# Performance work log

Hardware: AMD Instinct MI355X
Metric: run time of the kernel (lower is better)

## Reference

```python
import jax, jax.numpy as jnp
import numpy as np

EPS = 1e-5  # BatchNorm1d default eps
HEADS = 4


def _batchnorm(x, gamma, beta):
    # BatchNorm1d applied per graph: stats over node axis (axis=1), biased var (training mode)
    mean = x.mean(axis=1, keepdims=True)
    var = x.var(axis=1, keepdims=True)
    return gamma * (x - mean) * jax.lax.rsqrt(var + EPS) + beta


def setup_inputs() -> dict:
    key = jax.random.key(0)
    ks = jax.random.split(key, 8)
    B, N, F_in, C = 4, 4096, 128, 64
    inputs = jax.random.normal(ks[0], (B, N, F_in), jnp.float32)
    # sparse-ish adjacency (avg degree ~16); only used for non-emptiness check since conv=None
    adj = (jax.random.uniform(ks[1], (B, N, N)) < 0.004).astype(jnp.float32)
    s = lambda k, shp, fan: jax.random.normal(k, shp, jnp.float32) / np.sqrt(fan)
    return dict(
        inputs=inputs, adj=adj,
        Wp=s(ks[2], (C, F_in), F_in), bp=jnp.zeros((C,), jnp.float32),      # project Linear
        Wqkv=s(ks[3], (3 * C, C), C), bqkv=jnp.zeros((3 * C,), jnp.float32),  # MHA in_proj
        Wo=s(ks[4], (C, C), C), bo=jnp.zeros((C,), jnp.float32),            # MHA out_proj
        g2=jnp.ones((C,), jnp.float32), b2=jnp.zeros((C,), jnp.float32),    # norm2 (BatchNorm)
        W1=s(ks[5], (2 * C, C), C), b1=jnp.zeros((2 * C,), jnp.float32),    # MLP Linear 1
        W2=s(ks[6], (C, 2 * C), 2 * C), b2m=jnp.zeros((C,), jnp.float32),   # MLP Linear 2
        g3=jnp.ones((C,), jnp.float32), b3=jnp.zeros((C,), jnp.float32),    # norm3 (BatchNorm)
    )


def reference(inputs, adj, Wp, bp, Wqkv, bqkv, Wo, bo, g2, b2, W1, b1, W2, b2m, g3, b3):
    B, N, _ = inputs.shape
    C = Wp.shape[0]
    Dh = C // HEADS
    # project in_features -> out_features
    x = jnp.einsum('bnf,cf->bnc', inputs, Wp) + bp
    # GPSConv with conv=None: only the global multi-head self-attention branch runs
    qkv = jnp.einsum('bnc,dc->bnd', x, Wqkv) + bqkv
    q, k, v = jnp.split(qkv, 3, axis=-1)
    rs = lambda t: t.reshape(B, N, HEADS, Dh)
    q, k, v = rs(q), rs(k), rs(v)
    scores = jnp.einsum('bnhd,bmhd->bhnm', q, k) / np.sqrt(Dh).astype(np.float32)
    attn = jax.nn.softmax(scores, axis=-1)
    o = jnp.einsum('bhnm,bmhd->bnhd', attn, v).reshape(B, N, C)
    h = jnp.einsum('bnc,oc->bno', o, Wo) + bo
    # residual + norm2
    h = _batchnorm(h + x, g2, b2)
    # out = h (sum of single-branch hs); out = out + mlp(out); norm3
    mlp = jnp.einsum('bnk,ck->bnc',
                     jax.nn.relu(jnp.einsum('bnc,kc->bnk', h, W1) + b1),
                     W2) + b2m
    out = _batchnorm(h + mlp, g3, b3)
    # wrapper applies tanh (edge_index non-empty)
    return jnp.tanh(out)
```

## Files before the change

kernel.cpp:

```cpp
#include <hip/hip_runtime.h>
#include <hip/hip_bf16.h>

constexpr int NN = 4096;
constexpr int CC = 64;
constexpr int NH = 4;
constexpr int DH = 16;
constexpr int KSPLIT = 4;

typedef _Float16 f16x4 __attribute__((ext_vector_type(4)));
typedef float f32x4 __attribute__((ext_vector_type(4)));

#define QSCALE 0.36067376022224085f
#define L2E2   2.8853900817779268f

#if defined(__has_builtin)
#if __has_builtin(__builtin_amdgcn_exp2f)
#define FAST_EXP2(x) __builtin_amdgcn_exp2f(x)
#endif
#if __has_builtin(__builtin_amdgcn_rcpf)
#define FAST_RCP(x) __builtin_amdgcn_rcpf(x)
#endif
#endif
#ifndef FAST_EXP2
#define FAST_EXP2(x) exp2f(x)
#endif
#ifndef FAST_RCP
#define FAST_RCP(x) (1.0f / (x))
#endif

__device__ __forceinline__ float fast_tanh(float x) {
  const float t = FAST_EXP2(x * L2E2);
  return fmaf(-2.f, FAST_RCP(t + 1.f), 1.f);
}

__global__ __launch_bounds__(256) void proj_qkv_k(
    const float* __restrict__ inp, const float* __restrict__ Wp,
    const float* __restrict__ bp, const float* __restrict__ Wqkv,
    const float* __restrict__ bqkv, float* __restrict__ xout,
    _Float16* __restrict__ f16b)
{
  __shared__ __align__(16) float As[64][68];
  __shared__ __align__(16) float Xs[64][68];
  __shared__ __align__(16) float W2s[64][196];

  const int tid = threadIdx.x;
  const int rowbase = blockIdx.x * 64;
  const int r4 = (tid & 15) * 4;
  const int cg = (tid >> 4) * 4;
  const int cg2 = (tid >> 4) * 12;

  float acc[4][4];
  #pragma unroll
  for (int i = 0; i < 4; ++i)
    #pragma unroll
    for (int j = 0; j < 4; ++j) acc[i][j] = 0.f;

  for (int k0 = 0; k0 < 128; k0 += 64) {
    if (k0) __syncthreads();
    #pragma unroll
    for (int i = 0; i < 16; ++i) {
      int idx = tid + i * 256;
      int c2 = idx >> 6, kk = idx & 63;
      Xs[kk][c2] = Wp[(size_t)c2 * 128 + k0 + kk];
    }
    #pragma unroll
    for (int i = 0; i < 16; ++i) {
      int idx = tid + i * 256;
      int r = idx >> 6, kk = idx & 63;
      As[kk][r] = inp[(size_t)(rowbase + r) * 128 + k0 + kk];
    }
    __syncthreads();
    #pragma unroll 4
    for (int kk = 0; kk < 64; ++kk) {
      const float4 a = *(const float4*)&As[kk][r4];
      const float4 w4 = *(const float4*)&Xs[kk][cg];
      const float av[4] = {a.x, a.y, a.z, a.w};
      const float wv[4] = {w4.x, w4.y, w4.z, w4.w};
      #pragma unroll
      for (int ri = 0; ri < 4; ++ri)
        #pragma unroll
        for (int ci = 0; ci < 4; ++ci)
          acc[ri][ci] = fmaf(av[ri], wv[ci], acc[ri][ci]);
    }
  }

  float xv[4][4];
  #pragma unroll
  for (int ri = 0; ri < 4; ++ri)
    #pragma unroll
    for (int j = 0; j < 4; ++j) {
      xv[ri][j] = acc[ri][j] + bp[cg + j];
      xout[(size_t)(rowbase + r4 + ri) * CC + cg + j] = xv[ri][j];
    }

  __syncthreads();
  #pragma unroll
  for (int ri = 0; ri < 4; ++ri)
    #pragma unroll
    for (int j = 0; j < 4; ++j)
      Xs[cg + j][r4 + ri] = xv[ri][j];
  #pragma unroll
  for (int i = 0; i < 48; ++i) {
    int idx = tid + i * 256;
    int c2 = idx >> 6, kk = idx & 63;
    W2s[kk][c2] = Wqkv[(size_t)c2 * 64 + kk];
  }
  __syncthreads();

  float acc2[4][12];
  #pragma unroll
  for (int i = 0; i < 4; ++i)
    #pragma unroll
    for (int j = 0; j < 12; ++j) acc2[i][j] = 0.f;

  #pragma unroll 4
  for (int kk = 0; kk < 64; ++kk) {
    const float4 a = *(const float4*)&Xs[kk][r4];
    const float av[4] = {a.x, a.y, a.z, a.w};
    #pragma unroll
    for (int cj = 0; cj < 3; ++cj) {
      const float4 w4 = *(const float4*)&W2s[kk][cg2 + cj * 4];
      const float wv[4] = {w4.x, w4.y, w4.z, w4.w};
      #pragma unroll
      for (int ri = 0; ri < 4; ++ri)
        #pragma unroll
        for (int ci = 0; ci < 4; ++ci)
          acc2[ri][cj * 4 + ci] = fmaf(av[ri], wv[ci], acc2[ri][cj * 4 + ci]);
    }
  }

  #pragma unroll
  for (int ri = 0; ri < 4; ++ri) {
    const int row = rowbase + r4 + ri;
    const int n = row & (NN - 1);
    const int bq = (row >> 12) * NH;
    #pragma unroll
    for (int j = 0; j < 12; ++j) {
      float v = acc2[ri][j] + bqkv[cg2 + j];
      const int c2 = cg2 + j;
      const int which = c2 >> 6;
      const int hc = c2 & 63;
      const int bh = bq + (hc >> 4);
      const int d = hc & 15;
      if (which == 0) v *= QSCALE;
      if (which < 2)
        f16b[(size_t)which * 1048576 + ((size_t)bh * NN + n) * DH + d] = (_Float16)v;
      else
        f16b[2097152 + ((size_t)bh * DH + d) * NN + n] = (_Float16)v;
    }
  }
}

__global__ __launch_bounds__(256, 8) void attn_k(
    const _Float16* __restrict__ qb, const _Float16* __restrict__ kb,
    const _Float16* __restrict__ vtb, float* __restrict__ po,
    float* __restrict__ rs)
{
  __shared__ _Float16 Kl[64][20];
  __shared__ _Float16 Vl[16][72];

  const int bid = blockIdx.x;
  const int xcd = bid & 7;
  const int rest = bid >> 3;
  const int bh = 2 * xcd + (rest & 1);
  const int ks = (rest >> 1) & 3;
  const int n0 = (rest >> 3) * 128;
  const int tid = threadIdx.x;
  const int w = tid >> 6;
  const int l = tid & 63;
  const int g = l >> 4, i = l & 15;
  const int qbase = n0 + w * 32;
  const int kbeg = ks * (NN / KSPLIT);
  const int kend = kbeg + NN / KSPLIT;

  const _Float16* __restrict__ qhp = qb + (size_t)bh * NN * DH;
  const _Float16* __restrict__ khp = kb + (size_t)bh * NN * DH;
  const _Float16* __restrict__ vhp = vtb + (size_t)bh * DH * NN;

  const f16x4 qfA = *(const f16x4*)(qhp + (size_t)(qbase + i) * DH + 4 * g);
  const f16x4 qfB = *(const f16x4*)(qhp + (size_t)(qbase + 16 + i) * DH + 4 * g);

  f32x4 oA = {0.f, 0.f, 0.f, 0.f}, oB = {0.f, 0.f, 0.f, 0.f};
  const f32x4 zz = {0.f, 0.f, 0.f, 0.f};
  float rsA = 0.f, rsB = 0.f;

  const int srow = tid >> 2, spart = tid & 3;
  const int sd = tid >> 4, scol = (tid & 15) * 4;

  for (int c0 = kbeg; c0 < kend; c0 += 64) {
    __syncthreads();
    *(f16x4*)&Kl[srow][spart * 4] =
        *(const f16x4*)(khp + (size_t)(c0 + srow) * DH + spart * 4);
    *(f16x4*)&Vl[sd][scol] =
        *(const f16x4*)(vhp + (size_t)sd * NN + c0 + scol);
    __syncthreads();

    #pragma unroll
    for (int kk = 0; kk < 64; kk += 16) {
      const f16x4 kf = *(const f16x4*)&Kl[kk + i][4 * g];
      const f16x4 vf = *(const f16x4*)&Vl[i][kk + 4 * g];
      f32x4 sA = __builtin_amdgcn_mfma_f32_16x16x16f16(kf, qfA, zz, 0, 0, 0);
      f32x4 sB = __builtin_amdgcn_mfma_f32_16x16x16f16(kf, qfB, zz, 0, 0, 0);
      const float a0 = FAST_EXP2(sA[0]), a1 = FAST_EXP2(sA[1]),
                  a2 = FAST_EXP2(sA[2]), a3 = FAST_EXP2(sA[3]);
      const float b0 = FAST_EXP2(sB[0]), b1 = FAST_EXP2(sB[1]),
                  b2 = FAST_EXP2(sB[2]), b3 = FAST_EXP2(sB[3]);
      rsA += (a0 + a1) + (a2 + a3);
      rsB += (b0 + b1) + (b2 + b3);
      const auto alo = __builtin_amdgcn_cvt_pkrtz(a0, a1);
      const auto ahi = __builtin_amdgcn_cvt_pkrtz(a2, a3);
      const auto blo = __builtin_amdgcn_cvt_pkrtz(b0, b1);
      const auto bhi = __builtin_amdgcn_cvt_pkrtz(b2, b3);
      f16x4 pA, pB;
      pA[0] = (_Float16)alo[0]; pA[1] = (_Float16)alo[1];
      pA[2] = (_Float16)ahi[0]; pA[3] = (_Float16)ahi[1];
      pB[0] = (_Float16)blo[0]; pB[1] = (_Float16)blo[1];
      pB[2] = (_Float16)bhi[0]; pB[3] = (_Float16)bhi[1];
      oA = __builtin_amdgcn_mfma_f32_16x16x16f16(pA, vf, oA, 0, 0, 0);
      oB = __builtin_amdgcn_mfma_f32_16x16x16f16(pB, vf, oB, 0, 0, 0);
    }
  }

  rsA += __shfl_xor(rsA, 16); rsA += __shfl_xor(rsA, 32);
  rsB += __shfl_xor(rsB, 16); rsB += __shfl_xor(rsB, 32);

  float* __restrict__ pob = po + (size_t)(ks * 16 + bh) * NN * DH;
  #pragma unroll
  for (int r = 0; r < 4; ++r) {
    const int ql = 4 * g + r;
    pob[(size_t)(qbase + ql) * DH + i] = oA[r];
    pob[(size_t)(qbase + 16 + ql) * DH + i] = oB[r];
  }
  if (g == 0) {
    float* __restrict__ rsb = rs + (size_t)(ks * 16 + bh) * NN;
    rsb[qbase + i] = rsA;
    rsb[qbase + 16 + i] = rsB;
  }
}

__global__ __launch_bounds__(256) void wo_red_k(
    const float* __restrict__ po, const float* __restrict__ rs,
    const float* __restrict__ Wo, const float* __restrict__ bo,
    const float* __restrict__ xin, float* __restrict__ out)
{
  __shared__ __align__(16) float As[64][68];
  __shared__ __align__(16) float Ws[64][68];
  __shared__ float Linv[64][4];

  const int tid = threadIdx.x;
  const int rowbase = blockIdx.x * 64;
  const int r4 = (tid & 15) * 4;
  const int cg = (tid >> 4) * 4;

  {
    const int r = tid & 63, hb = tid >> 6;
    const int row = rowbase + r;
    const int bh = (row >> 12) * NH + hb;
    const int n = row & (NN - 1);
    const float s = rs[(size_t)bh * NN + n] + rs[(size_t)(16 + bh) * NN + n] +
                    rs[(size_t)(32 + bh) * NN + n] + rs[(size_t)(48 + bh) * NN + n];
    Linv[r][hb] = 1.f / s;
  }
  #pragma unroll
  for (int i = 0; i < 16; ++i) {
    int idx = tid + i * 256;
    int c2 = idx >> 6, kk = idx & 63;
    Ws[kk][c2] = Wo[(size_t)c2 * 64 + kk];
  }
  __syncthreads();
  #pragma unroll
  for (int i = 0; i < 16; ++i) {
    int idx = tid + i * 256;
    int r = idx >> 6, kk = idx & 63;
    const int row = rowbase + r;
    const int bh = (row >> 12) * NH + (kk >> 4);
    const int n = row & (NN - 1);
    const int d = kk & 15;
    const size_t base = (((size_t)bh * NN + n) * DH) + d;
    const float v = po[base] + po[base + 1048576] +
                    po[base + 2097152] + po[base + 3145728];
    As[kk][r] = v * Linv[r][kk >> 4];
  }
  __syncthreads();

  float acc[4][4];
  #pragma unroll
  for (int i = 0; i < 4; ++i)
    #pragma unroll
    for (int j = 0; j < 4; ++j) acc[i][j] = 0.f;

  #pragma unroll 4
  for (int kk = 0; kk < 64; ++kk) {
    const float4 a = *(const float4*)&As[kk][r4];
    const float4 w4 = *(const float4*)&Ws[kk][cg];
    const float av[4] = {a.x, a.y, a.z, a.w};
    const float wv[4] = {w4.x, w4.y, w4.z, w4.w};
    #pragma unroll
    for (int ri = 0; ri < 4; ++ri)
      #pragma unroll
      for (int ci = 0; ci < 4; ++ci)
        acc[ri][ci] = fmaf(av[ri], wv[ci], acc[ri][ci]);
  }

  #pragma unroll
  for (int ri = 0; ri < 4; ++ri) {
    const int row = rowbase + r4 + ri;
    #pragma unroll
    for (int j = 0; j < 4; ++j) {
      const int c = cg + j;
      out[(size_t)row * CC + c] =
          acc[ri][j] + bo[c] + xin[(size_t)row * CC + c];
    }
  }
}

__global__ __launch_bounds__(256) void mlp_k(
    const float* __restrict__ hf, const float* __restrict__ W1,
    const float* __restrict__ b1, const float* __restrict__ W2,
    const float* __restrict__ b2m, float* __restrict__ out)
{
  __shared__ __align__(16) float As[64][68];
  __shared__ __align__(16) float Wbuf[8704];
  __shared__ __align__(16) float Ts[128][68];

  const int tid = threadIdx.x;
  const int rowbase = blockIdx.x * 64;
  const int r4 = (tid & 15) * 4;
  const int cg8 = (tid >> 4) * 8;
  const int cg4 = (tid >> 4) * 4;

  #pragma unroll
  for (int i = 0; i < 32; ++i) {
    int idx = tid + i * 256;
    int c2 = idx >> 6, kk = idx & 63;
    Wbuf[kk * 132 + c2] = W1[(size_t)c2 * 64 + kk];
  }
  #pragma unroll
  for (int i = 0; i < 16; ++i) {
    int idx = tid + i * 256;
    int r = idx >> 6, kk = idx & 63;
    As[kk][r] = hf[(size_t)(rowbase + r) * CC + kk];
  }
  __syncthreads();

  float acc1[4][8];
  #pragma unroll
  for (int i = 0; i < 4; ++i)
    #pragma unroll
    for (int j = 0; j < 8; ++j) acc1[i][j] = 0.f;

  #pragma unroll 4
  for (int kk = 0; kk < 64; ++kk) {
    const float4 a = *(const float4*)&As[kk][r4];
    const float av[4] = {a.x, a.y, a.z, a.w};
    #pragma unroll
    for (int cj = 0; cj < 2; ++cj) {
      const float4 w4 = *(const float4*)&Wbuf[kk * 132 + cg8 + cj * 4];
      const float wv[4] = {w4.x, w4.y, w4.z, w4.w};
      #pragma unroll
      for (int ri = 0; ri < 4; ++ri)
        #pragma unroll
        for (int ci = 0; ci < 4; ++ci)
          acc1[ri][cj * 4 + ci] = fmaf(av[ri], wv[ci], acc1[ri][cj * 4 + ci]);
    }
  }
  #pragma unroll
  for (int ri = 0; ri < 4; ++ri)
    #pragma unroll
    for (int j = 0; j < 8; ++j)
      Ts[cg8 + j][r4 + ri] = fmaxf(acc1[ri][j] + b1[cg8 + j], 0.f);
  __syncthreads();

  #pragma unroll
  for (int i = 0; i < 32; ++i) {
    int idx = tid + i * 256;
    int c2 = idx >> 7, kk = idx & 127;
    Wbuf[kk * 68 + c2] = W2[(size_t)c2 * 128 + kk];
  }
  __syncthreads();

  float acc2[4][4];
  #pragma unroll
  for (int i = 0; i < 4; ++i)
    #pragma unroll
    for (int j = 0; j < 4; ++j) acc2[i][j] = 0.f;

  #pragma unroll 4
  for (int kk = 0; kk < 128; ++kk) {
    const float4 a = *(const float4*)&Ts[kk][r4];
    const float4 w4 = *(const float4*)&Wbuf[kk * 68 + cg4];
    const float av[4] = {a.x, a.y, a.z, a.w};
    const float wv[4] = {w4.x, w4.y, w4.z, w4.w};
    #pragma unroll
    for (int ri = 0; ri < 4; ++ri)
      #pragma unroll
      for (int ci = 0; ci < 4; ++ci)
        acc2[ri][ci] = fmaf(av[ri], wv[ci], acc2[ri][ci]);
  }

  #pragma unroll
  for (int ri = 0; ri < 4; ++ri) {
    const int row = rowbase + r4 + ri;
    #pragma unroll
    for (int j = 0; j < 4; ++j) {
      const int c = cg4 + j;
      out[(size_t)row * CC + c] = acc2[ri][j] + b2m[c] + As[c][r4 + ri];
    }
  }
}

__global__ __launch_bounds__(256) void bn4_k(
    const float* __restrict__ in, const float* __restrict__ g,
    const float* __restrict__ b, float* __restrict__ out, int do_tanh)
{
  const int bb = blockIdx.x >> 4;
  const int c4 = (blockIdx.x & 15) * 4;
  const float* __restrict__ base = in + (size_t)bb * NN * CC + c4;
  const int tid = threadIdx.x;

  float4 s = {0, 0, 0, 0}, sq = {0, 0, 0, 0};
  #pragma unroll
  for (int i = 0; i < 16; ++i) {
    const float4 v = *(const float4*)&base[(size_t)(tid + i * 256) * CC];
    s.x += v.x; s.y += v.y; s.z += v.z; s.w += v.w;
    sq.x = fmaf(v.x, v.x, sq.x); sq.y = fmaf(v.y, v.y, sq.y);
    sq.z = fmaf(v.z, v.z, sq.z); sq.w = fmaf(v.w, v.w, sq.w);
  }
  #pragma unroll
  for (int off = 32; off; off >>= 1) {
    s.x += __shfl_down(s.x, off); s.y += __shfl_down(s.y, off);
    s.z += __shfl_down(s.z, off); s.w += __shfl_down(s.w, off);
    sq.x += __shfl_down(sq.x, off); sq.y += __shfl_down(sq.y, off);
    sq.z += __shfl_down(sq.z, off); sq.w += __shfl_down(sq.w, off);
  }
  __shared__ float red[4][8];
  const int wv = tid >> 6;
  if ((tid & 63) == 0) {
    red[wv][0] = s.x; red[wv][1] = s.y; red[wv][2] = s.z; red[wv][3] = s.w;
    red[wv][4] = sq.x; red[wv][5] = sq.y; red[wv][6] = sq.z; red[wv][7] = sq.w;
  }
  __syncthreads();
  float scale[4], shift[4];
  #pragma unroll
  for (int j = 0; j < 4; ++j) {
    const float ts = red[0][j] + red[1][j] + red[2][j] + red[3][j];
    const float tq = red[0][4 + j] + red[1][4 + j] + red[2][4 + j] + red[3][4 + j];
    const float mean = ts * (1.f / NN);
    const float var = tq * (1.f / NN) - mean * mean;
    const float rstd = rsqrtf(var + 1e-5f);
    scale[j] = g[c4 + j] * rstd;
    shift[j] = b[c4 + j] - mean * scale[j];
  }
  float* __restrict__ ob = out + (size_t)bb * NN * CC + c4;
  #pragma unroll
  for (int i = 0; i < 16; ++i) {
    const size_t idx = (size_t)(tid + i * 256) * CC;
    const float4 v = *(const float4*)&base[idx];
    float4 o;
    o.x = v.x * scale[0] + shift[0];
    o.y = v.y * scale[1] + shift[1];
    o.z = v.z * scale[2] + shift[2];
    o.w = v.w * scale[3] + shift[3];
    if (do_tanh) {
      o.x = fast_tanh(o.x); o.y = fast_tanh(o.y);
      o.z = fast_tanh(o.z); o.w = fast_tanh(o.w);
    }
    *(float4*)&ob[idx] = o;
  }
}

extern "C" void kernel_launch(void* const* d_in, const int* in_sizes, int n_in,
                              void* d_out, int out_size, void* d_ws, size_t ws_size,
                              hipStream_t stream)
{
  const float* inp  = (const float*)d_in[0];
  const float* Wp   = (const float*)d_in[2];
  const float* bp   = (const float*)d_in[3];
  const float* Wqkv = (const float*)d_in[4];
  const float* bqkv = (const float*)d_in[5];
  const float* Wo   = (const float*)d_in[6];
  const float* bo   = (const float*)d_in[7];
  const float* g2   = (const float*)d_in[8];
  const float* b2   = (const float*)d_in[9];
  const float* W1   = (const float*)d_in[10];
  const float* b1   = (const float*)d_in[11];
  const float* W2   = (const float*)d_in[12];
  const float* b2m  = (const float*)d_in[13];
  const float* g3   = (const float*)d_in[14];
  const float* b3   = (const float*)d_in[15];

  float* w = (float*)d_ws;
  float* x    = w;
  float* qkvA = w + 1048576;
  float* hf   = w + 2621440;
  float* pf   = w + 3670016;
  float* poW  = w + 4718592;
  float* rsW  = w + 8912896;

  _Float16* f16b = (_Float16*)qkvA;

  proj_qkv_k<<<dim3(256), dim3(256), 0, stream>>>(inp, Wp, bp, Wqkv, bqkv, x, f16b);
  attn_k<<<dim3(2048), dim3(256), 0, stream>>>(f16b, f16b + 1048576,
                                               f16b + 2097152, poW, rsW);
  wo_red_k<<<dim3(256), dim3(256), 0, stream>>>(poW, rsW, Wo, bo, x, hf);
  bn4_k<<<dim3(64), dim3(256), 0, stream>>>(hf, g2, b2, hf, 0);
  mlp_k<<<dim3(256), dim3(256), 0, stream>>>(hf, W1, b1, W2, b2m, pf);
  bn4_k<<<dim3(64), dim3(256), 0, stream>>>(pf, g3, b3, (float*)d_out, 1);
}
```

Baseline: 127.9 us.

## Double-buffer K/V tiles in attention kernel with register prefetch and larger chunks

The attention kernel now stages K and V in two LDS buffers of 128 keys each. The next chunk is loaded from global memory into registers while the current chunk is computed, then written to the other buffer. This replaces the two barriers per 64-key chunk with one barrier per 128-key chunk and uses 16-byte loads. The cost is twice the shared memory and more live registers, which may lower occupancy under the launch bound of 8 blocks.

Measured after the change: 206.6 us. 1.62x slower.

```diff
diff --git a/kernel.cpp b/kernel.cpp
--- a/kernel.cpp
+++ b/kernel.cpp
@@ -6,8 +6,10 @@
 constexpr int NH = 4;
 constexpr int DH = 16;
 constexpr int KSPLIT = 4;
+constexpr int KVB = 128;
 
 typedef _Float16 f16x4 __attribute__((ext_vector_type(4)));
+typedef _Float16 f16x8 __attribute__((ext_vector_type(8)));
 typedef float f32x4 __attribute__((ext_vector_type(4)));
 
 #define QSCALE 0.36067376022224085f
@@ -156,8 +158,8 @@
     const _Float16* __restrict__ vtb, float* __restrict__ po,
     float* __restrict__ rs)
 {
-  __shared__ _Float16 Kl[64][20];
-  __shared__ _Float16 Vl[16][72];
+  __shared__ _Float16 Kl[2][KVB][20];
+  __shared__ _Float16 Vl[2][16][KVB + 8];
 
   const int bid = blockIdx.x;
   const int xcd = bid & 7;
@@ -171,7 +173,6 @@
   const int g = l >> 4, i = l & 15;
   const int qbase = n0 + w * 32;
   const int kbeg = ks * (NN / KSPLIT);
-  const int kend = kbeg + NN / KSPLIT;
 
   const _Float16* __restrict__ qhp = qb + (size_t)bh * NN * DH;
   const _Float16* __restrict__ khp = kb + (size_t)bh * NN * DH;
@@ -184,21 +185,31 @@
   const f32x4 zz = {0.f, 0.f, 0.f, 0.f};
   float rsA = 0.f, rsB = 0.f;
 
-  const int srow = tid >> 2, spart = tid & 3;
-  const int sd = tid >> 4, scol = (tid & 15) * 4;
-
-  for (int c0 = kbeg; c0 < kend; c0 += 64) {
-    __syncthreads();
-    *(f16x4*)&Kl[srow][spart * 4] =
-        *(const f16x4*)(khp + (size_t)(c0 + srow) * DH + spart * 4);
-    *(f16x4*)&Vl[sd][scol] =
-        *(const f16x4*)(vhp + (size_t)sd * NN + c0 + scol);
-    __syncthreads();
-
-    #pragma unroll
-    for (int kk = 0; kk < 64; kk += 16) {
-      const f16x4 kf = *(const f16x4*)&Kl[kk + i][4 * g];
-      const f16x4 vf = *(const f16x4*)&Vl[i][kk + 4 * g];
+  const int sr = tid >> 1, sh = (tid & 1) * 8;
+  const int sd = tid >> 4, sc = (tid & 15) * 8;
+
+  {
+    const f16x8 kr = *(const f16x8*)(khp + (size_t)(kbeg + sr) * DH + sh);
+    const f16x8 vr = *(const f16x8*)(vhp + (size_t)sd * NN + kbeg + sc);
+    *(f16x8*)&Kl[0][sr][sh] = kr;
+    *(f16x8*)&Vl[0][sd][sc] = vr;
+  }
+  __syncthreads();
+
+  constexpr int NCH = (NN / KSPLIT) / KVB;
+  int cur = 0;
+  for (int c = 0; c < NCH; ++c) {
+    f16x8 kr, vr;
+    if (c + 1 < NCH) {
+      const int nx = kbeg + (c + 1) * KVB;
+      kr = *(const f16x8*)(khp + (size_t)(nx + sr) * DH + sh);
+      vr = *(const f16x8*)(vhp + (size_t)sd * NN + nx + sc);
+    }
+
+    #pragma unroll
+    for (int kk = 0; kk < KVB; kk += 16) {
+      const f16x4 kf = *(const f16x4*)&Kl[cur][kk + i][4 * g];
+      const f16x4 vf = *(const f16x4*)&Vl[cur][i][kk + 4 * g];
       f32x4 sA = __builtin_amdgcn_mfma_f32_16x16x16f16(kf, qfA, zz, 0, 0, 0);
       f32x4 sB = __builtin_amdgcn_mfma_f32_16x16x16f16(kf, qfB, zz, 0, 0, 0);
       const float a0 = FAST_EXP2(sA[0]), a1 = FAST_EXP2(sA[1]),
@@ -219,6 +230,13 @@
       oA = __builtin_amdgcn_mfma_f32_16x16x16f16(pA, vf, oA, 0, 0, 0);
       oB = __builtin_amdgcn_mfma_f32_16x16x16f16(pB, vf, oB, 0, 0, 0);
     }
+
+    if (c + 1 < NCH) {
+      *(f16x8*)&Kl[cur ^ 1][sr][sh] = kr;
+      *(f16x8*)&Vl[cur ^ 1][sd][sc] = vr;
+    }
+    __syncthreads();
+    cur ^= 1;
   }
 
   rsA += __shfl_xor(rsA, 16); rsA += __shfl_xor(rsA, 32);
```

## Shrink GEMM row tiles to 16 rows and read weights from global cache

Applied to the files above, without the earlier changes.

The projection/QKV, Wo-reduce and MLP kernels now each handle 16 rows per block instead of 64. Each thread computes one row against a few output columns and reads weights directly from global memory through the cache, no longer staging them transposed in LDS. This launches 1024 blocks instead of 256, filling more of the GPU's compute units for these small GEMMs and cutting LDS use and staging syncs. The cost is less register reuse, more global/L1 weight reads per FMA, and uncoalesced row-strided input loads.

Result: slower. 192.3 us (+50.4%).

```diff
diff --git a/kernel.cpp b/kernel.cpp
--- a/kernel.cpp
+++ b/kernel.cpp
@@ -33,121 +33,68 @@
   return fmaf(-2.f, FAST_RCP(t + 1.f), 1.f);
 }
 
-__global__ __launch_bounds__(256) void proj_qkv_k(
+__global__ __launch_bounds__(256, 4) void proj_qkv_k(
     const float* __restrict__ inp, const float* __restrict__ Wp,
     const float* __restrict__ bp, const float* __restrict__ Wqkv,
     const float* __restrict__ bqkv, float* __restrict__ xout,
     _Float16* __restrict__ f16b)
 {
-  __shared__ __align__(16) float As[64][68];
-  __shared__ __align__(16) float Xs[64][68];
-  __shared__ __align__(16) float W2s[64][196];
-
-  const int tid = threadIdx.x;
-  const int rowbase = blockIdx.x * 64;
-  const int r4 = (tid & 15) * 4;
-  const int cg = (tid >> 4) * 4;
-  const int cg2 = (tid >> 4) * 12;
-
-  float acc[4][4];
-  #pragma unroll
-  for (int i = 0; i < 4; ++i)
-    #pragma unroll
-    for (int j = 0; j < 4; ++j) acc[i][j] = 0.f;
-
-  for (int k0 = 0; k0 < 128; k0 += 64) {
-    if (k0) __syncthreads();
-    #pragma unroll
-    for (int i = 0; i < 16; ++i) {
-      int idx = tid + i * 256;
-      int c2 = idx >> 6, kk = idx & 63;
-      Xs[kk][c2] = Wp[(size_t)c2 * 128 + k0 + kk];
-    }
-    #pragma unroll
-    for (int i = 0; i < 16; ++i) {
-      int idx = tid + i * 256;
-      int r = idx >> 6, kk = idx & 63;
-      As[kk][r] = inp[(size_t)(rowbase + r) * 128 + k0 + kk];
-    }
-    __syncthreads();
-    #pragma unroll 4
-    for (int kk = 0; kk < 64; ++kk) {
-      const float4 a = *(const float4*)&As[kk][r4];
-      const float4 w4 = *(const float4*)&Xs[kk][cg];
-      const float av[4] = {a.x, a.y, a.z, a.w};
-      const float wv[4] = {w4.x, w4.y, w4.z, w4.w};
-      #pragma unroll
-      for (int ri = 0; ri < 4; ++ri)
-        #pragma unroll
-        for (int ci = 0; ci < 4; ++ci)
-          acc[ri][ci] = fmaf(av[ri], wv[ci], acc[ri][ci]);
-    }
-  }
-
-  float xv[4][4];
-  #pragma unroll
-  for (int ri = 0; ri < 4; ++ri)
-    #pragma unroll
-    for (int j = 0; j < 4; ++j) {
-      xv[ri][j] = acc[ri][j] + bp[cg + j];
-      xout[(size_t)(rowbase + r4 + ri) * CC + cg + j] = xv[ri][j];
-    }
-
+  __shared__ __align__(16) float Xs[16][68];
+
+  const int tid = threadIdx.x;
+  const int rowbase = blockIdx.x * 16;
+  const int r = tid & 15;
+  const int cg = tid >> 4;
+  const int row = rowbase + r;
+
+  float acc[4] = {0.f, 0.f, 0.f, 0.f};
+  const float* arow = inp + (size_t)row * 128;
+  #pragma unroll 8
+  for (int k = 0; k < 128; k += 4) {
+    const float4 a = *(const float4*)(arow + k);
+    #pragma unroll
+    for (int ci = 0; ci < 4; ++ci) {
+      const float4 w = *(const float4*)(Wp + (size_t)(cg * 4 + ci) * 128 + k);
+      acc[ci] = fmaf(a.x, w.x, fmaf(a.y, w.y, fmaf(a.z, w.z, fmaf(a.w, w.w, acc[ci]))));
+    }
+  }
+  #pragma unroll
+  for (int ci = 0; ci < 4; ++ci) {
+    const float v = acc[ci] + bp[cg * 4 + ci];
+    xout[(size_t)row * CC + cg * 4 + ci] = v;
+    Xs[r][cg * 4 + ci] = v;
+  }
   __syncthreads();
-  #pragma unroll
-  for (int ri = 0; ri < 4; ++ri)
-    #pragma unroll
-    for (int j = 0; j < 4; ++j)
-      Xs[cg + j][r4 + ri] = xv[ri][j];
-  #pragma unroll
-  for (int i = 0; i < 48; ++i) {
-    int idx = tid + i * 256;
-    int c2 = idx >> 6, kk = idx & 63;
-    W2s[kk][c2] = Wqkv[(size_t)c2 * 64 + kk];
-  }
-  __syncthreads();
-
-  float acc2[4][12];
-  #pragma unroll
-  for (int i = 0; i < 4; ++i)
-    #pragma unroll
-    for (int j = 0; j < 12; ++j) acc2[i][j] = 0.f;
-
+
+  float acc2[12];
+  #pragma unroll
+  for (int j = 0; j < 12; ++j) acc2[j] = 0.f;
+  const int cg2 = cg * 12;
   #pragma unroll 4
-  for (int kk = 0; kk < 64; ++kk) {
-    const float4 a = *(const float4*)&Xs[kk][r4];
-    const float av[4] = {a.x, a.y, a.z, a.w};
-    #pragma unroll
-    for (int cj = 0; cj < 3; ++cj) {
-      const float4 w4 = *(const float4*)&W2s[kk][cg2 + cj * 4];
-      const float wv[4] = {w4.x, w4.y, w4.z, w4.w};
-      #pragma unroll
-      for (int ri = 0; ri < 4; ++ri)
-        #pragma unroll
-        for (int ci = 0; ci < 4; ++ci)
-          acc2[ri][cj * 4 + ci] = fmaf(av[ri], wv[ci], acc2[ri][cj * 4 + ci]);
-    }
-  }
-
-  #pragma unroll
-  for (int ri = 0; ri < 4; ++ri) {
-    const int row = rowbase + r4 + ri;
-    const int n = row & (NN - 1);
-    const int bq = (row >> 12) * NH;
+  for (int k = 0; k < 64; k += 4) {
+    const float4 a = *(const float4*)&Xs[r][k];
     #pragma unroll
     for (int j = 0; j < 12; ++j) {
-      float v = acc2[ri][j] + bqkv[cg2 + j];
-      const int c2 = cg2 + j;
-      const int which = c2 >> 6;
-      const int hc = c2 & 63;
-      const int bh = bq + (hc >> 4);
-      const int d = hc & 15;
-      if (which == 0) v *= QSCALE;
-      if (which < 2)
-        f16b[(size_t)which * 1048576 + ((size_t)bh * NN + n) * DH + d] = (_Float16)v;
-      else
-        f16b[2097152 + ((size_t)bh * DH + d) * NN + n] = (_Float16)v;
-    }
+      const float4 w = *(const float4*)(Wqkv + (size_t)(cg2 + j) * 64 + k);
+      acc2[j] = fmaf(a.x, w.x, fmaf(a.y, w.y, fmaf(a.z, w.z, fmaf(a.w, w.w, acc2[j]))));
+    }
+  }
+
+  const int n = row & (NN - 1);
+  const int bq = (row >> 12) * NH;
+  #pragma unroll
+  for (int j = 0; j < 12; ++j) {
+    float v = acc2[j] + bqkv[cg2 + j];
+    const int c2 = cg2 + j;
+    const int which = c2 >> 6;
+    const int hc = c2 & 63;
+    const int bh = bq + (hc >> 4);
+    const int d = hc & 15;
+    if (which == 0) v *= QSCALE;
+    if (which < 2)
+      f16b[(size_t)which * 1048576 + ((size_t)bh * NN + n) * DH + d] = (_Float16)v;
+    else
+      f16b[2097152 + ((size_t)bh * DH + d) * NN + n] = (_Float16)v;
   }
 }
 
@@ -238,174 +185,103 @@
   }
 }
 
-__global__ __launch_bounds__(256) void wo_red_k(
+__global__ __launch_bounds__(256, 4) void wo_red_k(
     const float* __restrict__ po, const float* __restrict__ rs,
     const float* __restrict__ Wo, const float* __restrict__ bo,
     const float* __restrict__ xin, float* __restrict__ out)
 {
-  __shared__ __align__(16) float As[64][68];
-  __shared__ __align__(16) float Ws[64][68];
-  __shared__ float Linv[64][4];
-
-  const int tid = threadIdx.x;
-  const int rowbase = blockIdx.x * 64;
-  const int r4 = (tid & 15) * 4;
-  const int cg = (tid >> 4) * 4;
+  __shared__ __align__(16) float Xs[16][68];
+
+  const int tid = threadIdx.x;
+  const int rowbase = blockIdx.x * 16;
 
   {
-    const int r = tid & 63, hb = tid >> 6;
+    const int r = tid >> 4, kk4 = (tid & 15) * 4;
     const int row = rowbase + r;
-    const int bh = (row >> 12) * NH + hb;
     const int n = row & (NN - 1);
-    const float s = rs[(size_t)bh * NN + n] + rs[(size_t)(16 + bh) * NN + n] +
-                    rs[(size_t)(32 + bh) * NN + n] + rs[(size_t)(48 + bh) * NN + n];
-    Linv[r][hb] = 1.f / s;
-  }
-  #pragma unroll
-  for (int i = 0; i < 16; ++i) {
-    int idx = tid + i * 256;
-    int c2 = idx >> 6, kk = idx & 63;
-    Ws[kk][c2] = Wo[(size_t)c2 * 64 + kk];
+    const int bh = (row >> 12) * NH + (kk4 >> 4);
+    const int d0 = kk4 & 15;
+    const size_t base = ((size_t)bh * NN + n) * DH + d0;
+    const float4 p0 = *(const float4*)(po + base);
+    const float4 p1 = *(const float4*)(po + base + 1048576);
+    const float4 p2 = *(const float4*)(po + base + 2097152);
+    const float4 p3 = *(const float4*)(po + base + 3145728);
+    const size_t rb = (size_t)bh * NN + n;
+    const float sden = rs[rb] + rs[rb + 65536] + rs[rb + 131072] + rs[rb + 196608];
+    const float inv = 1.f / sden;
+    Xs[r][kk4 + 0] = (p0.x + p1.x + p2.x + p3.x) * inv;
+    Xs[r][kk4 + 1] = (p0.y + p1.y + p2.y + p3.y) * inv;
+    Xs[r][kk4 + 2] = (p0.z + p1.z + p2.z + p3.z) * inv;
+    Xs[r][kk4 + 3] = (p0.w + p1.w + p2.w + p3.w) * inv;
   }
   __syncthreads();
-  #pragma unroll
-  for (int i = 0; i < 16; ++i) {
-    int idx = tid + i * 256;
-    int r = idx >> 6, kk = idx & 63;
-    const int row = rowbase + r;
-    const int bh = (row >> 12) * NH + (kk >> 4);
-    const int n = row & (NN - 1);
-    const int d = kk & 15;
-    const size_t base = (((size_t)bh * NN + n) * DH) + d;
-    const float v = po[base] + po[base + 1048576] +
-                    po[base + 2097152] + po[base + 3145728];
-    As[kk][r] = v * Linv[r][kk >> 4];
-  }
-  __syncthreads();
-
-  float acc[4][4];
-  #pragma unroll
-  for (int i = 0; i < 4; ++i)
-    #pragma unroll
-    for (int j = 0; j < 4; ++j) acc[i][j] = 0.f;
-
+
+  const int r = tid & 15;
+  const int cg = tid >> 4;
+  const int row = rowbase + r;
+  float acc[4] = {0.f, 0.f, 0.f, 0.f};
   #pragma unroll 4
-  for (int kk = 0; kk < 64; ++kk) {
-    const float4 a = *(const float4*)&As[kk][r4];
-    const float4 w4 = *(const float4*)&Ws[kk][cg];
-    const float av[4] = {a.x, a.y, a.z, a.w};
-    const float wv[4] = {w4.x, w4.y, w4.z, w4.w};
-    #pragma unroll
-    for (int ri = 0; ri < 4; ++ri)
-      #pragma unroll
-      for (int ci = 0; ci < 4; ++ci)
-        acc[ri][ci] = fmaf(av[ri], wv[ci], acc[ri][ci]);
-  }
-
-  #pragma unroll
-  for (int ri = 0; ri < 4; ++ri) {
-    const int row = rowbase + r4 + ri;
-    #pragma unroll
-    for (int j = 0; j < 4; ++j) {
-      const int c = cg + j;
-      out[(size_t)row * CC + c] =
-          acc[ri][j] + bo[c] + xin[(size_t)row * CC + c];
-    }
-  }
-}
-
-__global__ __launch_bounds__(256) void mlp_k(
+  for (int k = 0; k < 64; k += 4) {
+    const float4 a = *(const float4*)&Xs[r][k];
+    #pragma unroll
+    for (int ci = 0; ci < 4; ++ci) {
+      const float4 w = *(const float4*)(Wo + (size_t)(cg * 4 + ci) * 64 + k);
+      acc[ci] = fmaf(a.x, w.x, fmaf(a.y, w.y, fmaf(a.z, w.z, fmaf(a.w, w.w, acc[ci]))));
+    }
+  }
+  #pragma unroll
+  for (int ci = 0; ci < 4; ++ci) {
+    const int c = cg * 4 + ci;
+    out[(size_t)row * CC + c] = acc[ci] + bo[c] + xin[(size_t)row * CC + c];
+  }
+}
+
+__global__ __launch_bounds__(256, 4) void mlp_k(
     const float* __restrict__ hf, const float* __restrict__ W1,
     const float* __restrict__ b1, const float* __restrict__ W2,
     const float* __restrict__ b2m, float* __restrict__ out)
 {
-  __shared__ __align__(16) float As[64][68];
-  __shared__ __align__(16) float Wbuf[8704];
-  __shared__ __align__(16) float Ts[128][68];
-
-  const int tid = threadIdx.x;
-  const int rowbase = blockIdx.x * 64;
-  const int r4 = (tid & 15) * 4;
-  const int cg8 = (tid >> 4) * 8;
-  const int cg4 = (tid >> 4) * 4;
-
-  #pragma unroll
-  for (int i = 0; i < 32; ++i) {
-    int idx = tid + i * 256;
-    int c2 = idx >> 6, kk = idx & 63;
-    Wbuf[kk * 132 + c2] = W1[(size_t)c2 * 64 + kk];
-  }
-  #pragma unroll
-  for (int i = 0; i < 16; ++i) {
-    int idx = tid + i * 256;
-    int r = idx >> 6, kk = idx & 63;
-    As[kk][r] = hf[(size_t)(rowbase + r) * CC + kk];
-  }
+  __shared__ __align__(16) float Ts[16][132];
+
+  const int tid = threadIdx.x;
+  const int rowbase = blockIdx.x * 16;
+  const int r = tid & 15;
+  const int cg = tid >> 4;
+  const int row = rowbase + r;
+  const float* hrow = hf + (size_t)row * CC;
+
+  float acc1[8];
+  #pragma unroll
+  for (int j = 0; j < 8; ++j) acc1[j] = 0.f;
+  const int cg8 = cg * 8;
+  #pragma unroll 4
+  for (int k = 0; k < 64; k += 4) {
+    const float4 a = *(const float4*)(hrow + k);
+    #pragma unroll
+    for (int j = 0; j < 8; ++j) {
+      const float4 w = *(const float4*)(W1 + (size_t)(cg8 + j) * 64 + k);
+      acc1[j] = fmaf(a.x, w.x, fmaf(a.y, w.y, fmaf(a.z, w.z, fmaf(a.w, w.w, acc1[j]))));
+    }
+  }
+  #pragma unroll
+  for (int j = 0; j < 8; ++j)
+    Ts[r][cg8 + j] = fmaxf(acc1[j] + b1[cg8 + j], 0.f);
   __syncthreads();
 
-  float acc1[4][8];
-  #pragma unroll
-  for (int i = 0; i < 4; ++i)
-    #pragma unroll
-    for (int j = 0; j < 8; ++j) acc1[i][j] = 0.f;
-
+  float acc2[4] = {0.f, 0.f, 0.f, 0.f};
   #pragma unroll 4
-  for (int kk = 0; kk < 64; ++kk) {
-    const float4 a = *(const float4*)&As[kk][r4];
-    const float av[4] = {a.x, a.y, a.z, a.w};
-    #pragma unroll
-    for (int cj = 0; cj < 2; ++cj) {
-      const float4 w4 = *(const float4*)&Wbuf[kk * 132 + cg8 + cj * 4];
-      const float wv[4] = {w4.x, w4.y, w4.z, w4.w};
-      #pragma unroll
-      for (int ri = 0; ri < 4; ++ri)
-        #pragma unroll
-        for (int ci = 0; ci < 4; ++ci)
-          acc1[ri][cj * 4 + ci] = fmaf(av[ri], wv[ci], acc1[ri][cj * 4 + ci]);
-    }
-  }
-  #pragma unroll
-  for (int ri = 0; ri < 4; ++ri)
-    #pragma unroll
-    for (int j = 0; j < 8; ++j)
-      Ts[cg8 + j][r4 + ri] = fmaxf(acc1[ri][j] + b1[cg8 + j], 0.f);
-  __syncthreads();
-
-  #pragma unroll
-  for (int i = 0; i < 32; ++i) {
-    int idx = tid + i * 256;
-    int c2 = idx >> 7, kk = idx & 127;
-    Wbuf[kk * 68 + c2] = W2[(size_t)c2 * 128 + kk];
-  }
-  __syncthreads();
-
-  float acc2[4][4];
-  #pragma unroll
-  for (int i = 0; i < 4; ++i)
-    #pragma unroll
-    for (int j = 0; j < 4; ++j) acc2[i][j] = 0.f;
-
-  #pragma unroll 4
-  for (int kk = 0; kk < 128; ++kk) {
-    const float4 a = *(const float4*)&Ts[kk][r4];
-    const float4 w4 = *(const float4*)&Wbuf[kk * 68 + cg4];
-    const float av[4] = {a.x, a.y, a.z, a.w};
-    const float wv[4] = {w4.x, w4.y, w4.z, w4.w};
-    #pragma unroll
-    for (int ri = 0; ri < 4; ++ri)
-      #pragma unroll
-      for (int ci = 0; ci < 4; ++ci)
-        acc2[ri][ci] = fmaf(av[ri], wv[ci], acc2[ri][ci]);
-  }
-
-  #pragma unroll
-  for (int ri = 0; ri < 4; ++ri) {
-    const int row = rowbase + r4 + ri;
-    #pragma unroll
-    for (int j = 0; j < 4; ++j) {
-      const int c = cg4 + j;
-      out[(size_t)row * CC + c] = acc2[ri][j] + b2m[c] + As[c][r4 + ri];
-    }
+  for (int k = 0; k < 128; k += 4) {
+    const float4 a = *(const float4*)&Ts[r][k];
+    #pragma unroll
+    for (int ci = 0; ci < 4; ++ci) {
+      const float4 w = *(const float4*)(W2 + (size_t)(cg * 4 + ci) * 128 + k);
+      acc2[ci] = fmaf(a.x, w.x, fmaf(a.y, w.y, fmaf(a.z, w.z, fmaf(a.w, w.w, acc2[ci]))));
+    }
+  }
+  #pragma unroll
+  for (int ci = 0; ci < 4; ++ci) {
+    const int c = cg * 4 + ci;
+    out[(size_t)row * CC + c] = acc2[ci] + b2m[c] + hrow[c];
   }
 }
 
@@ -499,11 +375,11 @@
 
   _Float16* f16b = (_Float16*)qkvA;
 
-  proj_qkv_k<<<dim3(256), dim3(256), 0, stream>>>(inp, Wp, bp, Wqkv, bqkv, x, f16b);
+  proj_qkv_k<<<dim3(1024), dim3(256), 0, stream>>>(inp, Wp, bp, Wqkv, bqkv, x, f16b);
   attn_k<<<dim3(2048), dim3(256), 0, stream>>>(f16b, f16b + 1048576,
                                                f16b + 2097152, poW, rsW);
-  wo_red_k<<<dim3(256), dim3(256), 0, stream>>>(poW, rsW, Wo, bo, x, hf);
+  wo_red_k<<<dim3(1024), dim3(256), 0, stream>>>(poW, rsW, Wo, bo, x, hf);
   bn4_k<<<dim3(64), dim3(256), 0, stream>>>(hf, g2, b2, hf, 0);
-  mlp_k<<<dim3(256), dim3(256), 0, stream>>>(hf, W1, b1, W2, b2m, pf);
+  mlp_k<<<dim3(1024), dim3(256), 0, stream>>>(hf, W1, b1, W2, b2m, pf);
   bn4_k<<<dim3(64), dim3(256), 0, stream>>>(pf, g3, b3, (float*)d_out, 1);
 }
```

## Move attention key-split reduction inside block with per-wave private LDS tiles

Applied to the files above, without the earlier changes.

Each attention block now handles 32 queries, and its four waves each cover a quarter of the keys using private LDS tiles, so no block-wide barriers are needed in the key loop. The partial outputs and row sums are combined in shared memory and normalized, and the final per-head output is written directly in node-major layout. This removes the large fp32 partial-output and row-sum buffers and the four-way reduction in the Wo kernel. In exchange, each wave reloads K/V that the old design shared across four waves, which raises global/L2 traffic per query.

New measurement: 129.3 us. About the same (+1.1%).

```diff
diff --git a/kernel.cpp b/kernel.cpp
--- a/kernel.cpp
+++ b/kernel.cpp
@@ -5,9 +5,9 @@
 constexpr int CC = 64;
 constexpr int NH = 4;
 constexpr int DH = 16;
-constexpr int KSPLIT = 4;
 
 typedef _Float16 f16x4 __attribute__((ext_vector_type(4)));
+typedef _Float16 f16x8 __attribute__((ext_vector_type(8)));
 typedef float f32x4 __attribute__((ext_vector_type(4)));
 
 #define QSCALE 0.36067376022224085f
@@ -153,52 +153,50 @@
 
 __global__ __launch_bounds__(256, 8) void attn_k(
     const _Float16* __restrict__ qb, const _Float16* __restrict__ kb,
-    const _Float16* __restrict__ vtb, float* __restrict__ po,
-    float* __restrict__ rs)
+    const _Float16* __restrict__ vtb, float* __restrict__ of)
 {
-  __shared__ _Float16 Kl[64][20];
-  __shared__ _Float16 Vl[16][72];
+  __shared__ __align__(16) _Float16 KV[4][2176];
 
   const int bid = blockIdx.x;
   const int xcd = bid & 7;
   const int rest = bid >> 3;
   const int bh = 2 * xcd + (rest & 1);
-  const int ks = (rest >> 1) & 3;
-  const int n0 = (rest >> 3) * 128;
+  const int n0 = (rest >> 1) * 32;
   const int tid = threadIdx.x;
   const int w = tid >> 6;
   const int l = tid & 63;
   const int g = l >> 4, i = l & 15;
-  const int qbase = n0 + w * 32;
-  const int kbeg = ks * (NN / KSPLIT);
-  const int kend = kbeg + NN / KSPLIT;
+  const int kbeg = w * (NN / 4);
+
+  _Float16* __restrict__ Kl = &KV[w][0];
+  _Float16* __restrict__ Vl = &KV[w][1024];
 
   const _Float16* __restrict__ qhp = qb + (size_t)bh * NN * DH;
   const _Float16* __restrict__ khp = kb + (size_t)bh * NN * DH;
   const _Float16* __restrict__ vhp = vtb + (size_t)bh * DH * NN;
 
-  const f16x4 qfA = *(const f16x4*)(qhp + (size_t)(qbase + i) * DH + 4 * g);
-  const f16x4 qfB = *(const f16x4*)(qhp + (size_t)(qbase + 16 + i) * DH + 4 * g);
+  const f16x4 qfA = *(const f16x4*)(qhp + (size_t)(n0 + i) * DH + 4 * g);
+  const f16x4 qfB = *(const f16x4*)(qhp + (size_t)(n0 + 16 + i) * DH + 4 * g);
 
   f32x4 oA = {0.f, 0.f, 0.f, 0.f}, oB = {0.f, 0.f, 0.f, 0.f};
   const f32x4 zz = {0.f, 0.f, 0.f, 0.f};
   float rsA = 0.f, rsB = 0.f;
 
-  const int srow = tid >> 2, spart = tid & 3;
-  const int sd = tid >> 4, scol = (tid & 15) * 4;
-
-  for (int c0 = kbeg; c0 < kend; c0 += 64) {
-    __syncthreads();
-    *(f16x4*)&Kl[srow][spart * 4] =
-        *(const f16x4*)(khp + (size_t)(c0 + srow) * DH + spart * 4);
-    *(f16x4*)&Vl[sd][scol] =
-        *(const f16x4*)(vhp + (size_t)sd * NN + c0 + scol);
-    __syncthreads();
+  const int vrow = l >> 2, vcol = (l & 3) * 16;
+
+  for (int c0 = kbeg; c0 < kbeg + NN / 4; c0 += 64) {
+    #pragma unroll
+    for (int h = 0; h < 2; ++h) {
+      *(f16x8*)&Kl[l * 16 + h * 8] =
+          *(const f16x8*)(khp + (size_t)(c0 + l) * DH + h * 8);
+      *(f16x8*)&Vl[vrow * 72 + vcol + h * 8] =
+          *(const f16x8*)(vhp + (size_t)vrow * NN + c0 + vcol + h * 8);
+    }
 
     #pragma unroll
     for (int kk = 0; kk < 64; kk += 16) {
-      const f16x4 kf = *(const f16x4*)&Kl[kk + i][4 * g];
-      const f16x4 vf = *(const f16x4*)&Vl[i][kk + 4 * g];
+      const f16x4 kf = *(const f16x4*)&Kl[(kk + i) * 16 + 4 * g];
+      const f16x4 vf = *(const f16x4*)&Vl[i * 72 + kk + 4 * g];
       f32x4 sA = __builtin_amdgcn_mfma_f32_16x16x16f16(kf, qfA, zz, 0, 0, 0);
       f32x4 sB = __builtin_amdgcn_mfma_f32_16x16x16f16(kf, qfB, zz, 0, 0, 0);
       const float a0 = FAST_EXP2(sA[0]), a1 = FAST_EXP2(sA[1]),
@@ -224,62 +222,58 @@
   rsA += __shfl_xor(rsA, 16); rsA += __shfl_xor(rsA, 32);
   rsB += __shfl_xor(rsB, 16); rsB += __shfl_xor(rsB, 32);
 
-  float* __restrict__ pob = po + (size_t)(ks * 16 + bh) * NN * DH;
+  __syncthreads();
+  float* PO = (float*)&KV[0][0];
+  float* RS = PO + 2048;
   #pragma unroll
   for (int r = 0; r < 4; ++r) {
     const int ql = 4 * g + r;
-    pob[(size_t)(qbase + ql) * DH + i] = oA[r];
-    pob[(size_t)(qbase + 16 + ql) * DH + i] = oB[r];
+    PO[(w * 32 + ql) * 16 + i] = oA[r];
+    PO[(w * 32 + 16 + ql) * 16 + i] = oB[r];
   }
   if (g == 0) {
-    float* __restrict__ rsb = rs + (size_t)(ks * 16 + bh) * NN;
-    rsb[qbase + i] = rsA;
-    rsb[qbase + 16 + i] = rsB;
+    RS[w * 32 + i] = rsA;
+    RS[w * 32 + 16 + i] = rsB;
+  }
+  __syncthreads();
+
+  {
+    const int row = tid >> 3, d0 = (tid & 7) * 2;
+    const float s0 = PO[row * 16 + d0] + PO[(32 + row) * 16 + d0] +
+                     PO[(64 + row) * 16 + d0] + PO[(96 + row) * 16 + d0];
+    const float s1 = PO[row * 16 + d0 + 1] + PO[(32 + row) * 16 + d0 + 1] +
+                     PO[(64 + row) * 16 + d0 + 1] + PO[(96 + row) * 16 + d0 + 1];
+    const float inv = 1.f / (RS[row] + RS[32 + row] + RS[64 + row] + RS[96 + row]);
+    float* op = of + ((size_t)(bh >> 2) * NN + n0 + row) * CC + (bh & 3) * DH + d0;
+    op[0] = s0 * inv;
+    op[1] = s1 * inv;
   }
 }
 
 __global__ __launch_bounds__(256) void wo_red_k(
-    const float* __restrict__ po, const float* __restrict__ rs,
-    const float* __restrict__ Wo, const float* __restrict__ bo,
-    const float* __restrict__ xin, float* __restrict__ out)
+    const float* __restrict__ of, const float* __restrict__ Wo,
+    const float* __restrict__ bo, const float* __restrict__ xin,
+    float* __restrict__ out)
 {
   __shared__ __align__(16) float As[64][68];
   __shared__ __align__(16) float Ws[64][68];
-  __shared__ float Linv[64][4];
 
   const int tid = threadIdx.x;
   const int rowbase = blockIdx.x * 64;
   const int r4 = (tid & 15) * 4;
   const int cg = (tid >> 4) * 4;
 
-  {
-    const int r = tid & 63, hb = tid >> 6;
-    const int row = rowbase + r;
-    const int bh = (row >> 12) * NH + hb;
-    const int n = row & (NN - 1);
-    const float s = rs[(size_t)bh * NN + n] + rs[(size_t)(16 + bh) * NN + n] +
-                    rs[(size_t)(32 + bh) * NN + n] + rs[(size_t)(48 + bh) * NN + n];
-    Linv[r][hb] = 1.f / s;
-  }
   #pragma unroll
   for (int i = 0; i < 16; ++i) {
     int idx = tid + i * 256;
     int c2 = idx >> 6, kk = idx & 63;
     Ws[kk][c2] = Wo[(size_t)c2 * 64 + kk];
   }
-  __syncthreads();
   #pragma unroll
   for (int i = 0; i < 16; ++i) {
     int idx = tid + i * 256;
     int r = idx >> 6, kk = idx & 63;
-    const int row = rowbase + r;
-    const int bh = (row >> 12) * NH + (kk >> 4);
-    const int n = row & (NN - 1);
-    const int d = kk & 15;
-    const size_t base = (((size_t)bh * NN + n) * DH) + d;
-    const float v = po[base] + po[base + 1048576] +
-                    po[base + 2097152] + po[base + 3145728];
-    As[kk][r] = v * Linv[r][kk >> 4];
+    As[kk][r] = of[(size_t)(rowbase + r) * CC + kk];
   }
   __syncthreads();
 
@@ -494,16 +488,15 @@
   float* qkvA = w + 1048576;
   float* hf   = w + 2621440;
   float* pf   = w + 3670016;
-  float* poW  = w + 4718592;
-  float* rsW  = w + 8912896;
+  float* ofb  = w + 4718592;
 
   _Float16* f16b = (_Float16*)qkvA;
 
   proj_qkv_k<<<dim3(256), dim3(256), 0, stream>>>(inp, Wp, bp, Wqkv, bqkv, x, f16b);
   attn_k<<<dim3(2048), dim3(256), 0, stream>>>(f16b, f16b + 1048576,
-                                               f16b + 2097152, poW, rsW);
-  wo_red_k<<<dim3(256), dim3(256), 0, stream>>>(poW, rsW, Wo, bo, x, hf);
+                                               f16b + 2097152, ofb);
+  wo_red_k<<<dim3(256), dim3(256), 0, stream>>>(ofb, Wo, bo, x, hf);
   bn4_k<<<dim3(64), dim3(256), 0, stream>>>(hf, g2, b2, hf, 0);
-  mlp_k<<<dim3(256), dim3(256), 0, stream>>>(hf, W1, b1, W2, b2m, pf);
+  mlp_k<<<dim3(64 * 4), dim3(256), 0, stream>>>(hf, W1, b1, W2, b2m, pf);
   bn4_k<<<dim3(64), dim3(256), 0, stream>>>(pf, g3, b3, (float*)d_out, 1);
 }
```
